# Optimization experiments

Measured on AMD Instinct MI355X. Metric: run time of the kernel, lower is better.

Reference implementation:

```python
import jax, jax.numpy as jnp
import numpy as np

BITS = 4
MAXQ = (1 << BITS) - 1      # 15
PACK = 32 // BITS           # 8 values per int32 word
GROUP = 128                 # quantization group size along K


def setup_inputs() -> dict:
    key = jax.random.key(0)
    k0, k1, k2, k3 = jax.random.split(key, 4)
    M, K, N = 4096, 4096, 11008
    G = K // GROUP
    x = jax.random.normal(k0, (M, K), dtype=jnp.float32)
    # packed 4-bit weights: full-range random int32 words (each holds 8 nibbles)
    qweight = jax.random.randint(k1, (K // PACK, N), -(2**31), 2**31 - 1, dtype=jnp.int32)
    # packed zero points: (G, N // PACK) int32 words
    qzeros = jax.random.randint(k2, (G, N // PACK), -(2**31), 2**31 - 1, dtype=jnp.int32)
    # group-wise scales (G, N), small positive values as GPTQ produces
    scales = jax.random.uniform(k3, (G, N), dtype=jnp.float32, minval=1e-3, maxval=1e-2)
    # standard GPTQ grouping: consecutive blocks of GROUP rows share a group
    g_idx = (jnp.arange(K) // GROUP).astype(jnp.int32)
    return {"x": x, "qweight": qweight, "scales": scales, "qzeros": qzeros, "g_idx": g_idx}


def _dequant(qweight, scales, qzeros, g_idx):
    """Unpack int32-packed 4-bit weights and dequantize to float. Returns (K, N)."""
    K = g_idx.shape[0]
    N = qweight.shape[1]
    k = jnp.arange(K)
    # nibble k lives in word k//PACK at bit offset (k%PACK)*BITS
    k_shift = ((k % PACK) * BITS).astype(jnp.int32)
    w = (qweight[k // PACK] >> k_shift[:, None]) & MAXQ              # (K, N) int32 in [0, MAXQ]
    n = jnp.arange(N)
    n_shift = ((n % PACK) * BITS).astype(jnp.int32)
    z = ((qzeros[:, n // PACK] >> n_shift[None, :]) & MAXQ) + 1      # (G, N); kernel adds 1
    return (w - z[g_idx]).astype(scales.dtype) * scales[g_idx]       # (K, N) float


def reference(x, qweight, scales, qzeros, g_idx):
    # C = A @ dequant(B), fp32 accumulation as in the Triton kernel
    W = _dequant(qweight, scales, qzeros, g_idx)
    return jnp.matmul(x, W, preferred_element_type=jnp.float32)
```

## Files before the change

kernel.cpp:

```cpp
#include <hip/hip_runtime.h>
#include <hip/hip_bf16.h>
#include <stdint.h>

typedef _Float16 half8 __attribute__((ext_vector_type(8)));
typedef __attribute__((ext_vector_type(8))) short short8;
typedef __attribute__((ext_vector_type(4))) float floatx4;
typedef __attribute__((ext_vector_type(4))) uint32_t uint32x4;

#define GROUP_SZ 128

__device__ __forceinline__ uint32_t cvt_pk_f16(float lo, float hi) {
    uint32_t r;
    asm("v_cvt_pkrtz_f16_f32 %0, %1, %2" : "=v"(r) : "v"(lo), "v"(hi));
    return r;
}
__device__ __forceinline__ uint32_t pk_add_f16(uint32_t a, uint32_t b) {
    uint32_t r;
    asm("v_pk_add_f16 %0, %1, %2" : "=v"(r) : "v"(a), "v"(b));
    return r;
}
__device__ __forceinline__ uint32_t pk_mul_f16(uint32_t a, uint32_t b) {
    uint32_t r;
    asm("v_pk_mul_f16 %0, %1, %2" : "=v"(r) : "v"(a), "v"(b));
    return r;
}

__global__ __launch_bounds__(256)
void convA_kernel(const float* __restrict__ x, uint4* __restrict__ aws, int total8) {
    int idx = blockIdx.x * 256 + threadIdx.x;
    if (idx >= total8) return;
    const float4* xp = reinterpret_cast<const float4*>(x) + (size_t)idx * 2;
    float4 a = xp[0], b = xp[1];
    uint4 o;
    o.x = cvt_pk_f16(a.x, a.y);
    o.y = cvt_pk_f16(a.z, a.w);
    o.z = cvt_pk_f16(b.x, b.y);
    o.w = cvt_pk_f16(b.z, b.w);
    aws[idx] = o;
}

__global__ __launch_bounds__(256)
void deqB_kernel(const int* __restrict__ qw, const float* __restrict__ sc,
                 const int* __restrict__ qz, char* __restrict__ bws, int K, int N) {
    const int n = blockIdx.x * 256 + threadIdx.x;
    const int wk = blockIdx.y;
    if (n >= N) return;
    const uint32_t w = (uint32_t)qw[(size_t)wk * N + n];
    const int g = wk >> 4;
    const float s = sc[(size_t)g * N + n];
    const uint32_t zw = (uint32_t)qz[(size_t)g * (N >> 3) + (n >> 3)];
    const float zf = -(float)(1025u + ((zw >> ((n & 7) * 4)) & 15u));
    const uint32_t c2 = cvt_pk_f16(zf, zf);
    const uint32_t s2 = cvt_pk_f16(s, s);
    uint32_t oo[4];
    #pragma unroll
    for (int i = 0; i < 4; ++i) {
        const uint32_t tt = w >> (8 * i);
        const uint32_t qi = ((tt & 0xFu) | 0x64006400u) | ((tt << 12) & 0xF0000u);
        oo[i] = pk_mul_f16(pk_add_f16(qi, c2), s2);
    }
    uint4 o; o.x = oo[0]; o.y = oo[1]; o.z = oo[2]; o.w = oo[3];
    const int NKT = K >> 6;
    const int nt = n >> 8, h = (n >> 7) & 1, row = n & 127;
    const int kt = wk >> 3, slot = wk & 7;
    size_t off = ((((size_t)nt * NKT + kt) * 2 + h) * 8 + slot) * 2048 + (size_t)row * 16;
    *reinterpret_cast<uint4*>(bws + off) = o;
}

__global__ __launch_bounds__(512, 2)
void gemm8_kernel(const char* __restrict__ Aws, const char* __restrict__ Bws,
                  float* __restrict__ out, int M, int K, int N) {
    __shared__ char smem[131072];

    const int NT = K >> 6;
    const int nbm = M >> 8, nbn = N >> 8;
    const int nwg = nbm * nbn;
    int bid = blockIdx.x;
    int q = nwg >> 3, r = nwg & 7;
    int xcd = bid & 7, lin = bid >> 3;
    int sid = (xcd < r ? xcd * (q + 1) : r * (q + 1) + (xcd - r) * q) + lin;
    const int bm = sid / nbn, bn = sid % nbn;
    const int m0 = bm << 8, n0 = bn << 8;

    const int tid = threadIdx.x;
    const int lane = tid & 63, w = tid >> 6;
    const int wm = w >> 2, wn = w & 3;
    const int fr = lane & 15, hi = lane >> 4;
    const int r8 = lane >> 3, c8 = lane & 7;

    const size_t K2 = (size_t)K * 2;
    const char* aSrc[2][2];
    #pragma unroll
    for (int h = 0; h < 2; ++h)
        #pragma unroll
        for (int i = 0; i < 2; ++i)
            aSrc[h][i] = Aws + (size_t)(m0 + h * 128 + w * 16 + i * 8 + r8) * K2
                             + (size_t)((c8 ^ r8) * 16);
    const char* bSrc = Bws + (size_t)bn * ((size_t)NT * 32768)
                           + (size_t)w * 2048 + (size_t)lane * 16;

    auto stageA = [&](uint32_t buf, int h, int kt) {
        #pragma unroll
        for (int i = 0; i < 2; ++i) {
            const char* src = aSrc[h][i] + (size_t)kt * 128;
            char* dst = smem + buf * 65536u + (uint32_t)h * 16384u
                             + (uint32_t)w * 2048u + (uint32_t)i * 1024u;
            __builtin_amdgcn_global_load_lds(
                (const __attribute__((address_space(1))) void*)src,
                (__attribute__((address_space(3))) void*)dst, 16, 0, 0);
        }
    };
    auto stageB = [&](uint32_t buf, int h, int kt) {
        #pragma unroll
        for (int i = 0; i < 2; ++i) {
            const char* src = bSrc + ((size_t)kt * 2 + h) * 16384 + (size_t)i * 1024;
            char* dst = smem + buf * 65536u + 32768u + (uint32_t)h * 16384u
                             + (uint32_t)w * 2048u + (uint32_t)i * 1024u;
            __builtin_amdgcn_global_load_lds(
                (const __attribute__((address_space(1))) void*)src,
                (__attribute__((address_space(3))) void*)dst, 16, 0, 0);
        }
    };

    floatx4 acc[8][4];
    const floatx4 fz = {0.f, 0.f, 0.f, 0.f};
    #pragma unroll
    for (int i = 0; i < 8; ++i)
        #pragma unroll
        for (int j = 0; j < 4; ++j) acc[i][j] = fz;
    half8 af[4][2];
    half8 bf[2][2][2];

#define LOAD_AF(QM) { _Pragma("unroll") for (int fmi = 0; fmi < 4; ++fmi) { \
    _Pragma("unroll") for (int kk = 0; kk < 2; ++kk) { \
        uint32_t row = (uint32_t)(wm * 128 + ((QM) * 4 + fmi) * 16 + fr); \
        uint32_t p = (uint32_t)((kk * 4 + hi) ^ (fr & 7)); \
        uint32x4 u = *reinterpret_cast<const uint32x4*>(As + row * 128u + p * 16u); \
        af[fmi][kk] = __builtin_bit_cast(half8, u); } } }

#define LOAD_BF(QN) { _Pragma("unroll") for (int fnj = 0; fnj < 2; ++fnj) { \
    _Pragma("unroll") for (int kk = 0; kk < 2; ++kk) { \
        uint32_t nl = (uint32_t)(wn * 64 + ((QN) * 2 + fnj) * 16 + fr); \
        uint32_t off = (nl >> 7) * 16384u + (uint32_t)(kk * 4 + hi) * 2048u + (nl & 127u) * 16u; \
        uint32x4 u = *reinterpret_cast<const uint32x4*>(Bs + off); \
        bf[QN][fnj][kk] = __builtin_bit_cast(half8, u); } } }

#define MM(QM, QN) { _Pragma("unroll") for (int fmi = 0; fmi < 4; ++fmi) \
    _Pragma("unroll") for (int fnj = 0; fnj < 2; ++fnj) \
    _Pragma("unroll") for (int kk = 0; kk < 2; ++kk) \
        acc[(QM) * 4 + fmi][(QN) * 2 + fnj] = __builtin_amdgcn_mfma_f32_16x16x32_f16( \
            af[fmi][kk], bf[QN][fnj][kk], acc[(QM) * 4 + fmi][(QN) * 2 + fnj], 0, 0, 0); }

    stageA(0, 0, 0); stageA(0, 1, 0); stageB(0, 0, 0); stageB(0, 1, 0);
    if (NT > 1) { stageA(1, 0, 1); stageA(1, 1, 1); }
    asm volatile("s_waitcnt vmcnt(4)" ::: "memory");
    __builtin_amdgcn_s_barrier();

    for (int t = 0; t < NT; ++t) {
        const uint32_t c = (uint32_t)(t & 1), nb = c ^ 1u;
        const char* As = smem + c * 65536u;
        const char* Bs = As + 32768u;
        const bool st1 = (t + 1 < NT);
        const bool st2 = (t + 2 < NT);
        LOAD_AF(0); LOAD_BF(0);
        if (st1) stageB(nb, 0, t + 1);
        __builtin_amdgcn_s_barrier();
        __builtin_amdgcn_s_setprio(1); MM(0, 0); __builtin_amdgcn_s_setprio(0);
        __builtin_amdgcn_s_barrier();
        LOAD_BF(1);
        if (st1) stageB(nb, 1, t + 1);
        __builtin_amdgcn_s_barrier();
        __builtin_amdgcn_s_setprio(1); MM(0, 1); __builtin_amdgcn_s_setprio(0);
        __builtin_amdgcn_s_barrier();
        LOAD_AF(1);
        __builtin_amdgcn_s_barrier();
        __builtin_amdgcn_s_setprio(1); MM(1, 0); __builtin_amdgcn_s_setprio(0);
        __builtin_amdgcn_s_barrier();
        __builtin_amdgcn_sched_barrier(0);
        if (st2) { stageA(c, 0, t + 2); stageA(c, 1, t + 2); }
        __builtin_amdgcn_s_barrier();
        __builtin_amdgcn_s_setprio(1); MM(1, 1); __builtin_amdgcn_s_setprio(0);
        if (st2) {
            asm volatile("s_waitcnt vmcnt(4)" ::: "memory");
        } else if (st1) {
            asm volatile("s_waitcnt vmcnt(0)" ::: "memory");
        }
        if (st1) __builtin_amdgcn_s_barrier();
    }
#undef LOAD_AF
#undef LOAD_BF
#undef MM

    float* op = out + (size_t)(m0 + wm * 128) * N + n0 + wn * 64;
    #pragma unroll
    for (int fm = 0; fm < 8; ++fm)
        #pragma unroll
        for (int fn = 0; fn < 4; ++fn)
            #pragma unroll
            for (int rr = 0; rr < 4; ++rr)
                op[(size_t)(fm * 16 + hi * 4 + rr) * N + fn * 16 + fr] = acc[fm][fn][rr];
}

__device__ __forceinline__ uint32_t cvt_pk_bf16(float lo, float hi) {
    uint32_t r;
    asm("v_cvt_pk_bf16_f32 %0, %1, %2" : "=v"(r) : "v"(lo), "v"(hi));
    return r;
}
__device__ __forceinline__ uint32_t fswz(uint32_t row, uint32_t byte_in_row) {
    return row * 128u + (byte_in_row ^ ((row & 7u) << 4));
}

__global__ __launch_bounds__(256, 2)
void fused128_kernel(const float* __restrict__ x, const int* __restrict__ qweight,
                     const float* __restrict__ scales, const int* __restrict__ qzeros,
                     float* __restrict__ out, int M, int K, int N) {
    __shared__ char smem[32768];
    char* Ald = smem;
    char* Bld = smem + 16384;
    const int nbm = M / 128, nbn = N / 128;
    const int nwg = nbm * nbn;
    int bid = blockIdx.x;
    int q = nwg >> 3, r = nwg & 7;
    int xcd = bid & 7, lin = bid >> 3;
    int sid = (xcd < r ? xcd * (q + 1) : r * (q + 1) + (xcd - r) * q) + lin;
    int bm = sid / nbn, bn = sid % nbn;
    const int m0 = bm * 128, n0 = bn * 128;
    const int t = threadIdx.x;
    const int lane = t & 63, wave = t >> 6;
    const int tm = t >> 4, tk4 = t & 15;
    const int sn = t & 127, kwh = t >> 7;
    const int gn = n0 + sn;
    const int NT = K / 64;
    float4 av[8]; uint32_t qw[4]; float sc; uint32_t zw;
    const float* xp = x + (size_t)(m0 + tm) * K + tk4 * 4;
    const int* qp = qweight + (size_t)(kwh * 4) * N + gn;
    auto load_tile = [&](int ts) {
        const int k0 = ts * 64;
        #pragma unroll
        for (int i = 0; i < 8; ++i)
            av[i] = *reinterpret_cast<const float4*>(xp + (size_t)i * 16 * K + k0);
        const int g = k0 >> 7;
        sc = scales[(size_t)g * N + gn];
        zw = (uint32_t)qzeros[(size_t)g * (N >> 3) + (gn >> 3)];
        const int* qb = qp + (size_t)(k0 >> 3) * N;
        #pragma unroll
        for (int j = 0; j < 4; ++j) qw[j] = (uint32_t)qb[(size_t)j * N];
    };
    const int zsh = (gn & 7) * 4;
    auto write_tile = [&]() {
        #pragma unroll
        for (int i = 0; i < 8; ++i) {
            uint2 p;
            p.x = cvt_pk_bf16(av[i].x, av[i].y);
            p.y = cvt_pk_bf16(av[i].z, av[i].w);
            *reinterpret_cast<uint2*>(Ald + fswz((uint32_t)(i * 16 + tm), (uint32_t)(tk4 * 8))) = p;
        }
        const float z = (float)((zw >> zsh) & 15u) + 1.0f;
        const float nz = -z * sc;
        #pragma unroll
        for (int j = 0; j < 4; ++j) {
            const uint32_t wv = qw[j];
            float f[8];
            #pragma unroll
            for (int e = 0; e < 8; ++e)
                f[e] = fmaf((float)((wv >> (4 * e)) & 15u), sc, nz);
            uint4 p;
            p.x = cvt_pk_bf16(f[0], f[1]); p.y = cvt_pk_bf16(f[2], f[3]);
            p.z = cvt_pk_bf16(f[4], f[5]); p.w = cvt_pk_bf16(f[6], f[7]);
            *reinterpret_cast<uint4*>(Bld + fswz((uint32_t)sn, (uint32_t)((kwh * 4 + j) * 16))) = p;
        }
    };
    floatx4 acc[4][4];
    const floatx4 fz = {0.f, 0.f, 0.f, 0.f};
    #pragma unroll
    for (int i = 0; i < 4; ++i)
        #pragma unroll
        for (int j = 0; j < 4; ++j) acc[i][j] = fz;
    const int wm = (wave >> 1) * 64, wn = (wave & 1) * 64;
    const int fr = lane & 15;
    const int fkb = ((lane >> 4) * 8) * 2;
    auto compute = [&]() {
        #pragma unroll
        for (int kk = 0; kk < 2; ++kk) {
            short8 afv[4], bfv[4];
            #pragma unroll
            for (int i = 0; i < 4; ++i)
                afv[i] = *reinterpret_cast<const short8*>(
                    Ald + fswz((uint32_t)(wm + i * 16 + fr), (uint32_t)(kk * 64 + fkb)));
            #pragma unroll
            for (int i = 0; i < 4; ++i)
                bfv[i] = *reinterpret_cast<const short8*>(
                    Bld + fswz((uint32_t)(wn + i * 16 + fr), (uint32_t)(kk * 64 + fkb)));
            #pragma unroll
            for (int i = 0; i < 4; ++i)
                #pragma unroll
                for (int j = 0; j < 4; ++j)
                    acc[i][j] = __builtin_amdgcn_mfma_f32_16x16x32_bf16(afv[i], bfv[j], acc[i][j], 0, 0, 0);
        }
    };
    load_tile(0);
    write_tile();
    __syncthreads();
    for (int ts = 0; ts < NT; ++ts) {
        if (ts + 1 < NT) load_tile(ts + 1);
        compute();
        __syncthreads();
        if (ts + 1 < NT) write_tile();
        __syncthreads();
    }
    const int fq = lane >> 4;
    float* op = out + (size_t)(m0 + wm) * N + n0 + wn;
    #pragma unroll
    for (int i = 0; i < 4; ++i)
        #pragma unroll
        for (int j = 0; j < 4; ++j)
            #pragma unroll
            for (int rr = 0; rr < 4; ++rr)
                op[(size_t)(i * 16 + fq * 4 + rr) * N + j * 16 + fr] = acc[i][j][rr];
}

extern "C" void kernel_launch(void* const* d_in, const int* in_sizes, int n_in,
                              void* d_out, int out_size, void* d_ws, size_t ws_size,
                              hipStream_t stream) {
    const float* x       = (const float*)d_in[0];
    const int*   qweight = (const int*)d_in[1];
    const float* scales  = (const float*)d_in[2];
    const int*   qzeros  = (const int*)d_in[3];

    const int K = in_sizes[4];
    const int M = in_sizes[0] / K;
    const int G = K / GROUP_SZ;
    const int N = in_sizes[2] / G;
    float* out = (float*)d_out;

    const size_t needA = (size_t)M * K * 2;
    const size_t needB = (size_t)K * (size_t)N * 2;
    const bool ok = (ws_size >= needA + needB) && (M % 256 == 0) && (N % 256 == 0)
                    && (K % 128 == 0) && (N % 8 == 0);
    if (ok) {
        char* aws = (char*)d_ws;
        char* bws = aws + needA;
        const int total8 = M * (K / 8);
        hipLaunchKernelGGL(convA_kernel, dim3((total8 + 255) / 256), dim3(256), 0, stream,
                           x, (uint4*)aws, total8);
        hipLaunchKernelGGL(deqB_kernel, dim3((N + 255) / 256, K / 8), dim3(256), 0, stream,
                           qweight, scales, qzeros, bws, K, N);
        hipLaunchKernelGGL(gemm8_kernel, dim3((M / 256) * (N / 256)), dim3(512), 0, stream,
                           aws, bws, out, M, K, N);
    } else {
        const int nwg = (M / 128) * (N / 128);
        hipLaunchKernelGGL(fused128_kernel, dim3(nwg), dim3(256), 0, stream,
                           x, qweight, scales, qzeros, out, M, K, N);
    }
}
```

Measured before the change: 413.5 us.

## Software-pipeline MFMA quadrants across K iterations and use 32-bit address offsets

Reorders the per-iteration compute so the (1,1) quadrant MFMA of the previous K tile runs at the start of the next iteration, with double-buffered A/B fragment registers. Each LDS read then overlaps with a compute block, and the sched_barrier is removed. Global source addresses become a 64-bit base plus 32-bit offsets to cut 64-bit address arithmetic. The extra fragment registers raise register pressure, and the 32-bit offsets assume tile offsets fit in 32 bits.

```diff
diff --git a/kernel.cpp b/kernel.cpp
--- a/kernel.cpp
+++ b/kernel.cpp
@@ -88,21 +88,22 @@
     const int fr = lane & 15, hi = lane >> 4;
     const int r8 = lane >> 3, c8 = lane & 7;
 
-    const size_t K2 = (size_t)K * 2;
-    const char* aSrc[2][2];
+    const uint32_t K2 = (uint32_t)K * 2;
+    const char* aBase = Aws + (size_t)m0 * K2;
+    uint32_t aOff[2][2];
     #pragma unroll
     for (int h = 0; h < 2; ++h)
         #pragma unroll
         for (int i = 0; i < 2; ++i)
-            aSrc[h][i] = Aws + (size_t)(m0 + h * 128 + w * 16 + i * 8 + r8) * K2
-                             + (size_t)((c8 ^ r8) * 16);
-    const char* bSrc = Bws + (size_t)bn * ((size_t)NT * 32768)
-                           + (size_t)w * 2048 + (size_t)lane * 16;
+            aOff[h][i] = (uint32_t)(h * 128 + w * 16 + i * 8 + r8) * K2
+                       + (uint32_t)((c8 ^ r8) * 16);
+    const char* bBase = Bws + (size_t)bn * ((size_t)NT * 32768);
+    const uint32_t bOff = (uint32_t)w * 2048u + (uint32_t)lane * 16u;
 
     auto stageA = [&](uint32_t buf, int h, int kt) {
         #pragma unroll
         for (int i = 0; i < 2; ++i) {
-            const char* src = aSrc[h][i] + (size_t)kt * 128;
+            const char* src = aBase + aOff[h][i] + (uint32_t)kt * 128u;
             char* dst = smem + buf * 65536u + (uint32_t)h * 16384u
                              + (uint32_t)w * 2048u + (uint32_t)i * 1024u;
             __builtin_amdgcn_global_load_lds(
@@ -113,7 +114,7 @@
     auto stageB = [&](uint32_t buf, int h, int kt) {
         #pragma unroll
         for (int i = 0; i < 2; ++i) {
-            const char* src = bSrc + ((size_t)kt * 2 + h) * 16384 + (size_t)i * 1024;
+            const char* src = bBase + bOff + (uint32_t)((kt * 2 + h) * 16384 + i * 1024);
             char* dst = smem + buf * 65536u + 32768u + (uint32_t)h * 16384u
                              + (uint32_t)w * 2048u + (uint32_t)i * 1024u;
             __builtin_amdgcn_global_load_lds(
@@ -128,28 +129,28 @@
     for (int i = 0; i < 8; ++i)
         #pragma unroll
         for (int j = 0; j < 4; ++j) acc[i][j] = fz;
-    half8 af[4][2];
-    half8 bf[2][2][2];
-
-#define LOAD_AF(QM) { _Pragma("unroll") for (int fmi = 0; fmi < 4; ++fmi) { \
+    half8 af_a[4][2], af_b[4][2];
+    half8 bf_x[2][2], bf_y[2][2];
+
+#define LOAD_AF(AF, QM) { _Pragma("unroll") for (int fmi = 0; fmi < 4; ++fmi) { \
     _Pragma("unroll") for (int kk = 0; kk < 2; ++kk) { \
         uint32_t row = (uint32_t)(wm * 128 + ((QM) * 4 + fmi) * 16 + fr); \
         uint32_t p = (uint32_t)((kk * 4 + hi) ^ (fr & 7)); \
         uint32x4 u = *reinterpret_cast<const uint32x4*>(As + row * 128u + p * 16u); \
-        af[fmi][kk] = __builtin_bit_cast(half8, u); } } }
-
-#define LOAD_BF(QN) { _Pragma("unroll") for (int fnj = 0; fnj < 2; ++fnj) { \
+        AF[fmi][kk] = __builtin_bit_cast(half8, u); } } }
+
+#define LOAD_BF(BF, QN) { _Pragma("unroll") for (int fnj = 0; fnj < 2; ++fnj) { \
     _Pragma("unroll") for (int kk = 0; kk < 2; ++kk) { \
         uint32_t nl = (uint32_t)(wn * 64 + ((QN) * 2 + fnj) * 16 + fr); \
         uint32_t off = (nl >> 7) * 16384u + (uint32_t)(kk * 4 + hi) * 2048u + (nl & 127u) * 16u; \
         uint32x4 u = *reinterpret_cast<const uint32x4*>(Bs + off); \
-        bf[QN][fnj][kk] = __builtin_bit_cast(half8, u); } } }
-
-#define MM(QM, QN) { _Pragma("unroll") for (int fmi = 0; fmi < 4; ++fmi) \
+        BF[fnj][kk] = __builtin_bit_cast(half8, u); } } }
+
+#define MM(AF, BF, QM, QN) { _Pragma("unroll") for (int fmi = 0; fmi < 4; ++fmi) \
     _Pragma("unroll") for (int fnj = 0; fnj < 2; ++fnj) \
     _Pragma("unroll") for (int kk = 0; kk < 2; ++kk) \
         acc[(QM) * 4 + fmi][(QN) * 2 + fnj] = __builtin_amdgcn_mfma_f32_16x16x32_f16( \
-            af[fmi][kk], bf[QN][fnj][kk], acc[(QM) * 4 + fmi][(QN) * 2 + fnj], 0, 0, 0); }
+            AF[fmi][kk], BF[fnj][kk], acc[(QM) * 4 + fmi][(QN) * 2 + fnj], 0, 0, 0); }
 
     stageA(0, 0, 0); stageA(0, 1, 0); stageB(0, 0, 0); stageB(0, 1, 0);
     if (NT > 1) { stageA(1, 0, 1); stageA(1, 1, 1); }
@@ -162,24 +163,25 @@
         const char* Bs = As + 32768u;
         const bool st1 = (t + 1 < NT);
         const bool st2 = (t + 2 < NT);
-        LOAD_AF(0); LOAD_BF(0);
+        LOAD_AF(af_a, 0); LOAD_BF(bf_x, 0);
         if (st1) stageB(nb, 0, t + 1);
         __builtin_amdgcn_s_barrier();
-        __builtin_amdgcn_s_setprio(1); MM(0, 0); __builtin_amdgcn_s_setprio(0);
-        __builtin_amdgcn_s_barrier();
-        LOAD_BF(1);
+        if (t > 0) {
+            __builtin_amdgcn_s_setprio(1); MM(af_b, bf_y, 1, 1); __builtin_amdgcn_s_setprio(0);
+        }
+        __builtin_amdgcn_s_barrier();
+        LOAD_AF(af_b, 1);
         if (st1) stageB(nb, 1, t + 1);
         __builtin_amdgcn_s_barrier();
-        __builtin_amdgcn_s_setprio(1); MM(0, 1); __builtin_amdgcn_s_setprio(0);
-        __builtin_amdgcn_s_barrier();
-        LOAD_AF(1);
-        __builtin_amdgcn_s_barrier();
-        __builtin_amdgcn_s_setprio(1); MM(1, 0); __builtin_amdgcn_s_setprio(0);
-        __builtin_amdgcn_s_barrier();
-        __builtin_amdgcn_sched_barrier(0);
+        __builtin_amdgcn_s_setprio(1); MM(af_a, bf_x, 0, 0); __builtin_amdgcn_s_setprio(0);
+        __builtin_amdgcn_s_barrier();
+        LOAD_BF(bf_y, 1);
+        __builtin_amdgcn_s_barrier();
+        __builtin_amdgcn_s_setprio(1); MM(af_b, bf_x, 1, 0); __builtin_amdgcn_s_setprio(0);
+        __builtin_amdgcn_s_barrier();
         if (st2) { stageA(c, 0, t + 2); stageA(c, 1, t + 2); }
         __builtin_amdgcn_s_barrier();
-        __builtin_amdgcn_s_setprio(1); MM(1, 1); __builtin_amdgcn_s_setprio(0);
+        __builtin_amdgcn_s_setprio(1); MM(af_a, bf_y, 0, 1); __builtin_amdgcn_s_setprio(0);
         if (st2) {
             asm volatile("s_waitcnt vmcnt(4)" ::: "memory");
         } else if (st1) {
@@ -187,6 +189,7 @@
         }
         if (st1) __builtin_amdgcn_s_barrier();
     }
+    __builtin_amdgcn_s_setprio(1); MM(af_b, bf_y, 1, 1); __builtin_amdgcn_s_setprio(0);
 #undef LOAD_AF
 #undef LOAD_BF
 #undef MM
```

New measurement: 412.2 us. No clear change (-0.3%).
